# Kernel optimization log

Measured on AMD Instinct MI355X. Metric: run time of the kernel, lower is better.

The kernel has to match this reference:

```python
import jax, jax.numpy as jnp
import numpy as np

N = 8192
E = 262144
NODE_IN = 128
EDGE_IN = 64
OUT = 128


def setup_inputs() -> dict:
    key = jax.random.key(0)
    k1, k2, k3, k4, k5 = jax.random.split(key, 5)
    x = jax.random.normal(k1, (N, NODE_IN), dtype=jnp.float32)
    edge_index = jax.random.randint(k2, (2, E), 0, N, dtype=jnp.int64)
    edge_attr = jax.random.normal(k3, (E, EDGE_IN), dtype=jnp.float32)
    W = jax.random.normal(k4, (OUT, NODE_IN), dtype=jnp.float32) / np.sqrt(NODE_IN)
    a = jax.random.normal(k5, (1, 2 * OUT + EDGE_IN), dtype=jnp.float32) / np.sqrt(2 * OUT + EDGE_IN)
    return {"x": x, "edge_index": edge_index, "edge_attr": edge_attr, "W": W, "a": a}


def reference(x, edge_index, edge_attr, W, a):
    # h = W(x): [N, out]
    h = x @ W.T
    src, dst = edge_index[0], edge_index[1]
    # per-edge concat [h_src, h_dst, edge_attr]: [E, 2*out + edge_in]
    a_input = jnp.concatenate([h[src], h[dst], edge_attr], axis=1)
    # e = leakyrelu(a(a_input)): [E]
    e = jax.nn.leaky_relu(a_input @ a.T, negative_slope=0.2).squeeze(-1)
    n = h.shape[0]
    # dense scatter into NxN (non-edges stay 0 and DO participate in softmax,
    # matching the original torch module)
    attention = jnp.zeros((n, n), dtype=x.dtype).at[src, dst].set(e)
    attention = jax.nn.softmax(attention, axis=1)
    # aggregate: [N, out]
    return attention @ h
```

## Files before the change

### kernel.cpp

```cpp
#include <hip/hip_runtime.h>

#define N_NODES 8192
#define N_EDGES 262144
#define CAP 128
#define BM 16
#define NB_GEMM 512
#define NEB2 1024
#define NSB 32

typedef float vf4 __attribute__((ext_vector_type(4)));

__device__ inline unsigned short f2bf(float f) {
    unsigned u = __float_as_uint(f);
    u += 0x7FFF + ((u >> 16) & 1);
    return (unsigned short)(u >> 16);
}

__global__ __launch_bounds__(512) void k_gemm(const float* __restrict__ x,
                                              const float* __restrict__ W,
                                              const float* __restrict__ a,
                                              unsigned short* __restrict__ h2,
                                              float* __restrict__ asrc,
                                              float* __restrict__ adst,
                                              float* __restrict__ Spart,
                                              int* __restrict__ counts) {
    __shared__ float wlds[128 * 128];
    __shared__ float xlds[BM * 128];
    __shared__ float csum_l[8 * 130];

    const int tid = threadIdx.x;
    const int tc = tid & 63;
    const int tr = tid >> 6;
    const int r0 = blockIdx.x * BM;

    if (tid < BM) counts[blockIdx.x * BM + tid] = 0;

    {
        const int row = tid >> 5, k4 = (tid & 31) << 2;
        const vf4 v = __builtin_nontemporal_load(
            reinterpret_cast<const vf4*>(&x[(size_t)(r0 + row) * 128 + k4]));
        *reinterpret_cast<vf4*>(&xlds[row * 128 + k4]) = v;
    }
    #pragma unroll
    for (int i = tid; i < 4096; i += 512) {
        const int wr = i >> 5, k4 = (i & 31) << 2;
        const int ks = k4 ^ (((wr >> 1) & 31) << 2);
        *reinterpret_cast<float4*>(&wlds[wr * 128 + ks]) =
            *reinterpret_cast<const float4*>(&W[(size_t)wr * 128 + k4]);
    }
    __syncthreads();

    float acc[2][2] = {};
    const int R0 = 2 * tc;
    const int sw = (tc & 31) << 2;
    #pragma unroll 8
    for (int k0 = 0; k0 < 128; k0 += 4) {
        const int ks = k0 ^ sw;
        const float4 w0 = *reinterpret_cast<const float4*>(&wlds[R0 * 128 + ks]);
        const float4 w1 = *reinterpret_cast<const float4*>(&wlds[(R0 + 1) * 128 + ks]);
        #pragma unroll
        for (int r = 0; r < 2; ++r) {
            const float4 xv = *reinterpret_cast<const float4*>(&xlds[(2 * tr + r) * 128 + k0]);
            acc[r][0] += xv.x*w0.x + xv.y*w0.y + xv.z*w0.z + xv.w*w0.w;
            acc[r][1] += xv.x*w1.x + xv.y*w1.y + xv.z*w1.z + xv.w*w1.w;
        }
    }

    #pragma unroll
    for (int r = 0; r < 2; ++r) {
        ushort2 o; o.x = f2bf(acc[r][0]); o.y = f2bf(acc[r][1]);
        *reinterpret_cast<ushort2*>(&h2[(size_t)(r0 + 2 * tr + r) * 128 + 2 * tc]) = o;
    }
    {
        float2 cs;
        cs.x = acc[0][0] + acc[1][0];
        cs.y = acc[0][1] + acc[1][1];
        *reinterpret_cast<float2*>(&csum_l[tr * 130 + 2 * tc]) = cs;
    }

    const float a10 = a[2*tc], a11 = a[2*tc+1];
    const float a20 = a[128+2*tc], a21 = a[128+2*tc+1];
    #pragma unroll
    for (int r = 0; r < 2; ++r) {
        float v1 = acc[r][0]*a10 + acc[r][1]*a11;
        float v2 = acc[r][0]*a20 + acc[r][1]*a21;
        #pragma unroll
        for (int o = 32; o > 0; o >>= 1) { v1 += __shfl_down(v1, o); v2 += __shfl_down(v2, o); }
        if (tc == 0) { asrc[r0 + 2*tr + r] = v1; adst[r0 + 2*tr + r] = v2; }
    }
    __syncthreads();
    if (tid < 128) {
        float s = 0.f;
        #pragma unroll
        for (int gq = 0; gq < 8; ++gq) s += csum_l[gq * 130 + tid];
        Spart[(size_t)blockIdx.x * 128 + tid] = s;
    }
}

__global__ __launch_bounds__(256) void k_edge(const int* __restrict__ ei,
                                              const float* __restrict__ ea,
                                              const float* __restrict__ a,
                                              const float* __restrict__ asrc,
                                              const float* __restrict__ adst,
                                              int* __restrict__ counts,
                                              int2* __restrict__ bucket,
                                              const float* __restrict__ Spart,
                                              float* __restrict__ S) {
    const int blk = blockIdx.x;
    const int tid = threadIdx.x;
    if (blk >= NEB2) {
        const int c = (blk - NEB2) * 4 + (tid >> 6);
        const int l = tid & 63;
        float s = 0.f;
        #pragma unroll
        for (int j = 0; j < 8; ++j) s += Spart[(size_t)(l + 64 * j) * 128 + c];
        #pragma unroll
        for (int o = 32; o > 0; o >>= 1) s += __shfl_down(s, o);
        if (l == 0) S[c] = s;
        return;
    }
    __shared__ float d_l[256];
    const int lane16 = tid & 15;
    const int grp = tid >> 4;
    const int ebase = blk * 256;
    const int eid = ebase + tid;

    const int s = __builtin_nontemporal_load(&ei[eid]);
    const int t = __builtin_nontemporal_load(&ei[N_EDGES + eid]);
    const float as_ = asrc[s];
    const float at_ = adst[t];

    vf4 ev[16];
    #pragma unroll
    for (int p = 0; p < 16; ++p) {
        ev[p] = __builtin_nontemporal_load(
            reinterpret_cast<const vf4*>(&ea[(size_t)(ebase + p * 16 + grp) * 64 + lane16 * 4]));
    }
    const float4 av = *reinterpret_cast<const float4*>(&a[256 + lane16 * 4]);
    #pragma unroll
    for (int p = 0; p < 16; ++p) {
        float d = ev[p].x*av.x + ev[p].y*av.y + ev[p].z*av.z + ev[p].w*av.w;
        d += __shfl_xor(d, 1);
        d += __shfl_xor(d, 2);
        d += __shfl_xor(d, 4);
        d += __shfl_xor(d, 8);
        if (lane16 == 0) d_l[p * 16 + grp] = d;
    }
    __syncthreads();
    const float v = as_ + at_ + d_l[tid];
    const float ev_ = v > 0.f ? v : 0.2f * v;
    const int pos = atomicAdd(&counts[s], 1);
    if (pos < CAP) {
        int2 rec;
        rec.x = (int)(((unsigned)eid << 13) | (unsigned)t);
        rec.y = __float_as_int(ev_);
        bucket[(size_t)s * CAP + pos] = rec;
    }
}

__global__ __launch_bounds__(512) void k_row(const int2* __restrict__ bucket2,
                                             const int* __restrict__ counts,
                                             const unsigned short* __restrict__ h2,
                                             const float* __restrict__ S,
                                             float* __restrict__ out) {
    __shared__ __align__(16) int key_l[4][CAP];
    __shared__ float e_l[4][CAP];
    __shared__ float cw[4][CAP];
    __shared__ int cd[4][CAP];
    __shared__ float redm[4][2], reds[4][2];
    __shared__ int wcnt[4][2];
    __shared__ float4 xw[4][32];

    const int tid = threadIdx.x;
    const int sub = tid >> 7;
    const int t = tid & 127;
    const int lane = t & 63;
    const int wv = t >> 6;
    const int q = t & 31;
    const int g = t >> 5;
    const int row = blockIdx.x * 4 + sub;
    const float4 Sv4 = *reinterpret_cast<const float4*>(&S[4 * q]);

    int k = counts[row];
    if (k > CAP) k = CAP;
    const int kpad = (k + 3) & ~3;
    if (t < k) {
        const int2 rec = bucket2[(size_t)row * CAP + t];
        key_l[sub][t] = rec.x;
        e_l[sub][t] = __int_as_float(rec.y);
    } else if (t < kpad) {
        key_l[sub][t] = -1;
    }
    __syncthreads();

    bool win = false;
    float mloc = 0.f;
    if (t < k) {
        const int key = key_l[sub][t];
        win = true;
        for (int s2 = 0; s2 < kpad; s2 += 4) {
            const int4 kv = *reinterpret_cast<const int4*>(&key_l[sub][s2]);
            const bool hit = (((kv.x ^ key) & 8191) == 0 && kv.x > key)
                          || (((kv.y ^ key) & 8191) == 0 && kv.y > key)
                          || (((kv.z ^ key) & 8191) == 0 && kv.z > key)
                          || (((kv.w ^ key) & 8191) == 0 && kv.w > key);
            win = win && !hit;
        }
        if (win) { const float evv = e_l[sub][t]; mloc = evv > 0.f ? evv : 0.f; }
    }
    const unsigned long long wmask = __ballot(win);
    const int pos_in_wave = (int)__popcll(wmask & ((1ull << lane) - 1ull));
    if (lane == 0) wcnt[sub][wv] = (int)__popcll(wmask);
    #pragma unroll
    for (int o = 32; o > 0; o >>= 1) mloc = fmaxf(mloc, __shfl_down(mloc, o));
    if (lane == 0) redm[sub][wv] = mloc;
    __syncthreads();

    const float m = fmaxf(redm[sub][0], redm[sub][1]);
    const int nw = wcnt[sub][0] + wcnt[sub][1];
    const float w0 = expf(-m);
    float w = 0.f;
    if (win) {
        w = expf(e_l[sub][t] - m);
        const int p = (wv ? wcnt[sub][0] : 0) + pos_in_wave;
        cd[sub][p] = key_l[sub][t] & 8191;
        cw[sub][p] = w - w0;
    }
    float sloc = w;
    #pragma unroll
    for (int o = 32; o > 0; o >>= 1) sloc += __shfl_down(sloc, o);
    if (lane == 0) reds[sub][wv] = sloc;
    __syncthreads();
    const float D = (float)(N_NODES - nw) * w0 + reds[sub][0] + reds[sub][1];

    float4 acc0 = {0.f,0.f,0.f,0.f}, acc1 = {0.f,0.f,0.f,0.f};
    float4 acc2 = {0.f,0.f,0.f,0.f}, acc3 = {0.f,0.f,0.f,0.f};
    int j = g;
    for (; j + 12 < nw; j += 16) {
        const float c0 = cw[sub][j],      c1 = cw[sub][j + 4];
        const float c2 = cw[sub][j + 8],  c3 = cw[sub][j + 12];
        const int d0 = cd[sub][j],     d1 = cd[sub][j + 4];
        const int d2 = cd[sub][j + 8], d3 = cd[sub][j + 12];
        const ushort4 u0 = *reinterpret_cast<const ushort4*>(&h2[(size_t)d0 * 128 + 4 * q]);
        const ushort4 u1 = *reinterpret_cast<const ushort4*>(&h2[(size_t)d1 * 128 + 4 * q]);
        const ushort4 u2 = *reinterpret_cast<const ushort4*>(&h2[(size_t)d2 * 128 + 4 * q]);
        const ushort4 u3 = *reinterpret_cast<const ushort4*>(&h2[(size_t)d3 * 128 + 4 * q]);
        acc0.x += c0 * __uint_as_float((unsigned)u0.x << 16);
        acc0.y += c0 * __uint_as_float((unsigned)u0.y << 16);
        acc0.z += c0 * __uint_as_float((unsigned)u0.z << 16);
        acc0.w += c0 * __uint_as_float((unsigned)u0.w << 16);
        acc1.x += c1 * __uint_as_float((unsigned)u1.x << 16);
        acc1.y += c1 * __uint_as_float((unsigned)u1.y << 16);
        acc1.z += c1 * __uint_as_float((unsigned)u1.z << 16);
        acc1.w += c1 * __uint_as_float((unsigned)u1.w << 16);
        acc2.x += c2 * __uint_as_float((unsigned)u2.x << 16);
        acc2.y += c2 * __uint_as_float((unsigned)u2.y << 16);
        acc2.z += c2 * __uint_as_float((unsigned)u2.z << 16);
        acc2.w += c2 * __uint_as_float((unsigned)u2.w << 16);
        acc3.x += c3 * __uint_as_float((unsigned)u3.x << 16);
        acc3.y += c3 * __uint_as_float((unsigned)u3.y << 16);
        acc3.z += c3 * __uint_as_float((unsigned)u3.z << 16);
        acc3.w += c3 * __uint_as_float((unsigned)u3.w << 16);
    }
    for (; j < nw; j += 4) {
        const float c0 = cw[sub][j];
        const ushort4 u0 = *reinterpret_cast<const ushort4*>(&h2[(size_t)cd[sub][j] * 128 + 4 * q]);
        acc0.x += c0 * __uint_as_float((unsigned)u0.x << 16);
        acc0.y += c0 * __uint_as_float((unsigned)u0.y << 16);
        acc0.z += c0 * __uint_as_float((unsigned)u0.z << 16);
        acc0.w += c0 * __uint_as_float((unsigned)u0.w << 16);
    }
    float4 acc4;
    acc4.x = (acc0.x + acc1.x) + (acc2.x + acc3.x);
    acc4.y = (acc0.y + acc1.y) + (acc2.y + acc3.y);
    acc4.z = (acc0.z + acc1.z) + (acc2.z + acc3.z);
    acc4.w = (acc0.w + acc1.w) + (acc2.w + acc3.w);
    acc4.x += __shfl_down(acc4.x, 32);
    acc4.y += __shfl_down(acc4.y, 32);
    acc4.z += __shfl_down(acc4.z, 32);
    acc4.w += __shfl_down(acc4.w, 32);
    if (t >= 64 && t < 96) xw[sub][q] = acc4;
    __syncthreads();
    if (t < 32) {
        const float4 tt = xw[sub][q];
        float4 o;
        o.x = (w0 * Sv4.x + acc4.x + tt.x) / D;
        o.y = (w0 * Sv4.y + acc4.y + tt.y) / D;
        o.z = (w0 * Sv4.z + acc4.z + tt.z) / D;
        o.w = (w0 * Sv4.w + acc4.w + tt.w) / D;
        *reinterpret_cast<float4*>(&out[(size_t)row * 128 + 4 * q]) = o;
    }
}

extern "C" void kernel_launch(void* const* d_in, const int* in_sizes, int n_in,
                              void* d_out, int out_size, void* d_ws, size_t ws_size,
                              hipStream_t stream) {
    const float* x = (const float*)d_in[0];
    const int* ei = (const int*)d_in[1];
    const float* ea = (const float*)d_in[2];
    const float* W = (const float*)d_in[3];
    const float* a = (const float*)d_in[4];
    float* out = (float*)d_out;

    char* ws = (char*)d_ws;
    unsigned short* h2 = (unsigned short*)(ws);
    int2* bucket = (int2*)(ws + (2 << 20));
    float* Spart = (float*)(ws + (10 << 20));
    float* asrc = (float*)(ws + (10 << 20) + 262144);
    float* adst = (float*)(ws + (10 << 20) + 294912);
    int* counts = (int*)(ws + (10 << 20) + 327680);
    float* S = (float*)(ws + (10 << 20) + 360448);

    k_gemm<<<NB_GEMM, 512, 0, stream>>>(x, W, a, h2, asrc, adst, Spart, counts);
    k_edge<<<NEB2 + NSB, 256, 0, stream>>>(ei, ea, a, asrc, adst, counts, bucket, Spart, S);
    k_row<<<N_NODES / 4, 512, 0, stream>>>(bucket, counts, h2, S, out);
}
```

Baseline: 58.52 us.

## Split per-row edge buckets into 8 sub-buckets to reduce atomic contention

After: 63.37 us. 1.08x slower.

```diff
diff --git a/kernel.cpp b/kernel.cpp
--- a/kernel.cpp
+++ b/kernel.cpp
@@ -3,6 +3,7 @@
 #define N_NODES 8192
 #define N_EDGES 262144
 #define CAP 128
+#define CAPS 32
 #define BM 16
 #define NB_GEMM 512
 #define NEB2 1024
@@ -23,7 +24,7 @@
                                               float* __restrict__ asrc,
                                               float* __restrict__ adst,
                                               float* __restrict__ Spart,
-                                              int* __restrict__ counts) {
+                                              int* __restrict__ counts_all) {
     __shared__ float wlds[128 * 128];
     __shared__ float xlds[BM * 128];
     __shared__ float csum_l[8 * 130];
@@ -33,7 +34,7 @@
     const int tr = tid >> 6;
     const int r0 = blockIdx.x * BM;
 
-    if (tid < BM) counts[blockIdx.x * BM + tid] = 0;
+    counts_all[blockIdx.x * 512 + tid] = 0;
 
     {
         const int row = tid >> 5, k4 = (tid & 31) << 2;
@@ -102,8 +103,8 @@
                                               const float* __restrict__ a,
                                               const float* __restrict__ asrc,
                                               const float* __restrict__ adst,
-                                              int* __restrict__ counts,
-                                              int2* __restrict__ bucket,
+                                              int* __restrict__ counts_all,
+                                              int2* __restrict__ bucket_all,
                                               const float* __restrict__ Spart,
                                               float* __restrict__ S) {
     const int blk = blockIdx.x;
@@ -120,6 +121,10 @@
         return;
     }
     __shared__ float d_l[256];
+    const int g = blk & 7;
+    int* counts = counts_all + g * N_NODES;
+    int2* bucket = bucket_all + (size_t)g * N_NODES * CAPS;
+
     const int lane16 = tid & 15;
     const int grp = tid >> 4;
     const int ebase = blk * 256;
@@ -130,16 +135,13 @@
     const float as_ = asrc[s];
     const float at_ = adst[t];
 
-    vf4 ev[16];
-    #pragma unroll
+    const float4 av = *reinterpret_cast<const float4*>(&a[256 + lane16 * 4]);
+    #pragma unroll 4
     for (int p = 0; p < 16; ++p) {
-        ev[p] = __builtin_nontemporal_load(
-            reinterpret_cast<const vf4*>(&ea[(size_t)(ebase + p * 16 + grp) * 64 + lane16 * 4]));
-    }
-    const float4 av = *reinterpret_cast<const float4*>(&a[256 + lane16 * 4]);
-    #pragma unroll
-    for (int p = 0; p < 16; ++p) {
-        float d = ev[p].x*av.x + ev[p].y*av.y + ev[p].z*av.z + ev[p].w*av.w;
+        const int e2 = ebase + p * 16 + grp;
+        const vf4 ev = __builtin_nontemporal_load(
+            reinterpret_cast<const vf4*>(&ea[(size_t)e2 * 64 + lane16 * 4]));
+        float d = ev.x*av.x + ev.y*av.y + ev.z*av.z + ev.w*av.w;
         d += __shfl_xor(d, 1);
         d += __shfl_xor(d, 2);
         d += __shfl_xor(d, 4);
@@ -150,25 +152,26 @@
     const float v = as_ + at_ + d_l[tid];
     const float ev_ = v > 0.f ? v : 0.2f * v;
     const int pos = atomicAdd(&counts[s], 1);
-    if (pos < CAP) {
+    if (pos < CAPS) {
         int2 rec;
         rec.x = (int)(((unsigned)eid << 13) | (unsigned)t);
         rec.y = __float_as_int(ev_);
-        bucket[(size_t)s * CAP + pos] = rec;
-    }
-}
-
-__global__ __launch_bounds__(512) void k_row(const int2* __restrict__ bucket2,
-                                             const int* __restrict__ counts,
+        bucket[s * CAPS + pos] = rec;
+    }
+}
+
+__global__ __launch_bounds__(512) void k_row(const int2* __restrict__ bucket_all,
+                                             const int* __restrict__ counts_all,
                                              const unsigned short* __restrict__ h2,
                                              const float* __restrict__ S,
                                              float* __restrict__ out) {
-    __shared__ __align__(16) int key_l[4][CAP];
-    __shared__ float e_l[4][CAP];
+    __shared__ __align__(16) int key_l[4][136];
+    __shared__ float e_l[4][136];
     __shared__ float cw[4][CAP];
     __shared__ int cd[4][CAP];
     __shared__ float redm[4][2], reds[4][2];
     __shared__ int wcnt[4][2];
+    __shared__ int cnt8[4][8], off8[4][9];
     __shared__ float4 xw[4][32];
 
     const int tid = threadIdx.x;
@@ -181,16 +184,34 @@
     const int row = blockIdx.x * 4 + sub;
     const float4 Sv4 = *reinterpret_cast<const float4*>(&S[4 * q]);
 
-    int k = counts[row];
-    if (k > CAP) k = CAP;
+    if (t < 8) {
+        int c8 = counts_all[t * N_NODES + row];
+        cnt8[sub][t] = c8 > CAPS ? CAPS : c8;
+    }
+    __syncthreads();
+    if (t == 0) {
+        int o = 0;
+        #pragma unroll
+        for (int g2 = 0; g2 < 8; ++g2) { off8[sub][g2] = o; o += cnt8[sub][g2]; }
+        off8[sub][8] = o > CAP ? CAP : o;
+    }
+    __syncthreads();
+    const int k = off8[sub][8];
     const int kpad = (k + 3) & ~3;
-    if (t < k) {
-        const int2 rec = bucket2[(size_t)row * CAP + t];
-        key_l[sub][t] = rec.x;
-        e_l[sub][t] = __int_as_float(rec.y);
-    } else if (t < kpad) {
-        key_l[sub][t] = -1;
-    }
+    #pragma unroll
+    for (int pass = 0; pass < 2; ++pass) {
+        const int g2 = t >> 4;
+        const int j = (t & 15) + pass * 16;
+        if (j < cnt8[sub][g2]) {
+            const int p = off8[sub][g2] + j;
+            if (p < CAP) {
+                const int2 rec = bucket_all[((size_t)g2 * N_NODES + row) * CAPS + j];
+                key_l[sub][p] = rec.x;
+                e_l[sub][p] = __int_as_float(rec.y);
+            }
+        }
+    }
+    if (t < 3) key_l[sub][k + t] = -1;
     __syncthreads();
 
     bool win = false;
@@ -304,14 +325,14 @@
 
     char* ws = (char*)d_ws;
     unsigned short* h2 = (unsigned short*)(ws);
-    int2* bucket = (int2*)(ws + (2 << 20));
-    float* Spart = (float*)(ws + (10 << 20));
-    float* asrc = (float*)(ws + (10 << 20) + 262144);
-    float* adst = (float*)(ws + (10 << 20) + 294912);
-    int* counts = (int*)(ws + (10 << 20) + 327680);
-    float* S = (float*)(ws + (10 << 20) + 360448);
-
-    k_gemm<<<NB_GEMM, 512, 0, stream>>>(x, W, a, h2, asrc, adst, Spart, counts);
-    k_edge<<<NEB2 + NSB, 256, 0, stream>>>(ei, ea, a, asrc, adst, counts, bucket, Spart, S);
-    k_row<<<N_NODES / 4, 512, 0, stream>>>(bucket, counts, h2, S, out);
-}
+    int2* bucket_all = (int2*)(ws + (2 << 20));
+    float* Spart = (float*)(ws + (18 << 20));
+    float* asrc = (float*)(ws + (18 << 20) + 262144);
+    float* adst = (float*)(ws + (18 << 20) + 294912);
+    int* counts_all = (int*)(ws + (18 << 20) + 327680);
+    float* S = (float*)(ws + (18 << 20) + 589824);
+
+    k_gemm<<<NB_GEMM, 512, 0, stream>>>(x, W, a, h2, asrc, adst, Spart, counts_all);
+    k_edge<<<NEB2 + NSB, 256, 0, stream>>>(ei, ea, a, asrc, adst, counts_all, bucket_all, Spart, S);
+    k_row<<<N_NODES / 4, 512, 0, stream>>>(bucket_all, counts_all, h2, S, out);
+}
```

## Move edge-attribute dot product into GEMM kernel to overlap its streaming

Applied to the files above, without the earlier changes.

New measurement: 58.48 us. No clear change (-0.1%).

```diff
diff --git a/kernel.cpp b/kernel.cpp
--- a/kernel.cpp
+++ b/kernel.cpp
@@ -19,11 +19,13 @@
 __global__ __launch_bounds__(512) void k_gemm(const float* __restrict__ x,
                                               const float* __restrict__ W,
                                               const float* __restrict__ a,
+                                              const float* __restrict__ ea,
                                               unsigned short* __restrict__ h2,
                                               float* __restrict__ asrc,
                                               float* __restrict__ adst,
                                               float* __restrict__ Spart,
-                                              int* __restrict__ counts) {
+                                              int* __restrict__ counts,
+                                              float* __restrict__ d) {
     __shared__ float wlds[128 * 128];
     __shared__ float xlds[BM * 128];
     __shared__ float csum_l[8 * 130];
@@ -32,6 +34,9 @@
     const int tc = tid & 63;
     const int tr = tid >> 6;
     const int r0 = blockIdx.x * BM;
+    const int lane16 = tid & 15;
+    const int grp = tid >> 4;
+    const int ebase = blockIdx.x * 512;
 
     if (tid < BM) counts[blockIdx.x * BM + tid] = 0;
 
@@ -49,6 +54,14 @@
             *reinterpret_cast<const float4*>(&W[(size_t)wr * 128 + k4]);
     }
     __syncthreads();
+
+    vf4 ev[8];
+    #pragma unroll
+    for (int p = 0; p < 8; ++p) {
+        ev[p] = __builtin_nontemporal_load(
+            reinterpret_cast<const vf4*>(&ea[(size_t)(ebase + p * 32 + grp) * 64 + lane16 * 4]));
+    }
+    const float4 av = *reinterpret_cast<const float4*>(&a[256 + lane16 * 4]);
 
     float acc[2][2] = {};
     const int R0 = 2 * tc;
@@ -67,6 +80,21 @@
     }
 
     #pragma unroll
+    for (int p = 0; p < 8; ++p) {
+        float dv = ev[p].x*av.x + ev[p].y*av.y + ev[p].z*av.z + ev[p].w*av.w;
+        dv += __shfl_xor(dv, 1);
+        dv += __shfl_xor(dv, 2);
+        dv += __shfl_xor(dv, 4);
+        dv += __shfl_xor(dv, 8);
+        if (lane16 == 0) d[ebase + p * 32 + grp] = dv;
+    }
+    #pragma unroll
+    for (int p = 0; p < 8; ++p) {
+        ev[p] = __builtin_nontemporal_load(
+            reinterpret_cast<const vf4*>(&ea[(size_t)(ebase + (p + 8) * 32 + grp) * 64 + lane16 * 4]));
+    }
+
+    #pragma unroll
     for (int r = 0; r < 2; ++r) {
         ushort2 o; o.x = f2bf(acc[r][0]); o.y = f2bf(acc[r][1]);
         *reinterpret_cast<ushort2*>(&h2[(size_t)(r0 + 2 * tr + r) * 128 + 2 * tc]) = o;
@@ -95,11 +123,20 @@
         for (int gq = 0; gq < 8; ++gq) s += csum_l[gq * 130 + tid];
         Spart[(size_t)blockIdx.x * 128 + tid] = s;
     }
+
+    #pragma unroll
+    for (int p = 0; p < 8; ++p) {
+        float dv = ev[p].x*av.x + ev[p].y*av.y + ev[p].z*av.z + ev[p].w*av.w;
+        dv += __shfl_xor(dv, 1);
+        dv += __shfl_xor(dv, 2);
+        dv += __shfl_xor(dv, 4);
+        dv += __shfl_xor(dv, 8);
+        if (lane16 == 0) d[ebase + (p + 8) * 32 + grp] = dv;
+    }
 }
 
 __global__ __launch_bounds__(256) void k_edge(const int* __restrict__ ei,
-                                              const float* __restrict__ ea,
-                                              const float* __restrict__ a,
+                                              const float* __restrict__ d,
                                               const float* __restrict__ asrc,
                                               const float* __restrict__ adst,
                                               int* __restrict__ counts,
@@ -119,41 +156,16 @@
         if (l == 0) S[c] = s;
         return;
     }
-    __shared__ float d_l[256];
-    const int lane16 = tid & 15;
-    const int grp = tid >> 4;
-    const int ebase = blk * 256;
-    const int eid = ebase + tid;
-
+    const int eid = blk * 256 + tid;
     const int s = __builtin_nontemporal_load(&ei[eid]);
     const int t = __builtin_nontemporal_load(&ei[N_EDGES + eid]);
-    const float as_ = asrc[s];
-    const float at_ = adst[t];
-
-    vf4 ev[16];
-    #pragma unroll
-    for (int p = 0; p < 16; ++p) {
-        ev[p] = __builtin_nontemporal_load(
-            reinterpret_cast<const vf4*>(&ea[(size_t)(ebase + p * 16 + grp) * 64 + lane16 * 4]));
-    }
-    const float4 av = *reinterpret_cast<const float4*>(&a[256 + lane16 * 4]);
-    #pragma unroll
-    for (int p = 0; p < 16; ++p) {
-        float d = ev[p].x*av.x + ev[p].y*av.y + ev[p].z*av.z + ev[p].w*av.w;
-        d += __shfl_xor(d, 1);
-        d += __shfl_xor(d, 2);
-        d += __shfl_xor(d, 4);
-        d += __shfl_xor(d, 8);
-        if (lane16 == 0) d_l[p * 16 + grp] = d;
-    }
-    __syncthreads();
-    const float v = as_ + at_ + d_l[tid];
-    const float ev_ = v > 0.f ? v : 0.2f * v;
+    const float v = asrc[s] + adst[t] + d[eid];
+    const float ev = v > 0.f ? v : 0.2f * v;
     const int pos = atomicAdd(&counts[s], 1);
     if (pos < CAP) {
         int2 rec;
         rec.x = (int)(((unsigned)eid << 13) | (unsigned)t);
-        rec.y = __float_as_int(ev_);
+        rec.y = __float_as_int(ev);
         bucket[(size_t)s * CAP + pos] = rec;
     }
 }
@@ -305,13 +317,14 @@
     char* ws = (char*)d_ws;
     unsigned short* h2 = (unsigned short*)(ws);
     int2* bucket = (int2*)(ws + (2 << 20));
-    float* Spart = (float*)(ws + (10 << 20));
-    float* asrc = (float*)(ws + (10 << 20) + 262144);
-    float* adst = (float*)(ws + (10 << 20) + 294912);
-    int* counts = (int*)(ws + (10 << 20) + 327680);
-    float* S = (float*)(ws + (10 << 20) + 360448);
-
-    k_gemm<<<NB_GEMM, 512, 0, stream>>>(x, W, a, h2, asrc, adst, Spart, counts);
-    k_edge<<<NEB2 + NSB, 256, 0, stream>>>(ei, ea, a, asrc, adst, counts, bucket, Spart, S);
+    float* dbuf = (float*)(ws + (10 << 20));
+    float* Spart = (float*)(ws + (11 << 20));
+    float* asrc = (float*)(ws + (11 << 20) + 262144);
+    float* adst = (float*)(ws + (11 << 20) + 294912);
+    int* counts = (int*)(ws + (11 << 20) + 327680);
+    float* S = (float*)(ws + (11 << 20) + 360448);
+
+    k_gemm<<<NB_GEMM, 512, 0, stream>>>(x, W, a, ea, h2, asrc, adst, Spart, counts, dbuf);
+    k_edge<<<NEB2 + NSB, 256, 0, stream>>>(ei, dbuf, asrc, adst, counts, bucket, Spart, S);
     k_row<<<N_NODES / 4, 512, 0, stream>>>(bucket, counts, h2, S, out);
 }
```
